# Kernel optimization log

Hardware: AMD Instinct MI355X
Metric: run time of the kernel (lower is better)

The kernel has to match this reference:

```python
import jax, jax.numpy as jnp
import numpy as np

S, B, F = 2048, 2, 1024
H, D = 16, 64
P = H * D  # packed dim = 1024


def setup_inputs() -> dict:
    key = jax.random.key(0)
    k1, k2, k3 = jax.random.split(key, 3)
    return {
        "src": jax.random.normal(k1, (S, B, F), dtype=jnp.float32),
        "in_proj_weight": jax.random.normal(k2, (3 * P, F), dtype=jnp.float32) * (1.0 / np.sqrt(F)),
        "in_proj_bias": jnp.zeros((3 * P,), dtype=jnp.float32),
        "out_proj_weight": jax.random.normal(k3, (F, P), dtype=jnp.float32) * (1.0 / np.sqrt(P)),
        "out_proj_bias": jnp.zeros((F,), dtype=jnp.float32),
    }


def reference(src, in_proj_weight, in_proj_bias, out_proj_weight, out_proj_bias):
    s, b, f = src.shape
    h, d = H, D
    # fused QKV projection: [S,B,3P]
    qkv = jnp.einsum("sbf,pf->sbp", src, in_proj_weight) + in_proj_bias
    q, k, v = jnp.split(qkv, 3, axis=-1)  # each [S,B,P]
    # [S,B,P] -> [S, B*H, D] -> [B*H, S, D]
    def to_heads(x):
        return jnp.swapaxes(x.reshape(s, b * h, d), 0, 1)
    q = to_heads(q) / np.sqrt(d)
    k = to_heads(k)
    v = to_heads(v)
    attn = jnp.einsum("nsd,ntd->nst", q, k)  # [B*H, S, S]
    attn = jax.nn.softmax(attn, axis=-1)
    out = jnp.einsum("nst,ntd->nsd", attn, v)  # [B*H, S, D]
    out = jnp.swapaxes(out, 0, 1).reshape(s * b, h * d)  # [S*B, P]
    out = out @ out_proj_weight.T + out_proj_bias  # [S*B, F]
    return out.reshape(s, b, f)
```

## Files before the change

### kernel.cpp

```cpp
#include <hip/hip_runtime.h>

#define S_LEN 2048
#define B_SZ  2
#define F_DIM 1024
#define H_N   16
#define D_DIM 64
#define P_DIM 1024
#define M_ROWS 4096
#define NBH   32

typedef __bf16 bf16x8 __attribute__((ext_vector_type(8)));
typedef __bf16 bf16x4 __attribute__((ext_vector_type(4)));
typedef float  f32x4  __attribute__((ext_vector_type(4)));
typedef unsigned short u16;
typedef unsigned short u16x8 __attribute__((ext_vector_type(8)));
typedef unsigned short u16x4 __attribute__((ext_vector_type(4)));

__device__ __forceinline__ float bf2f(u16 u) {
  union { unsigned int i; float f; } x;
  x.i = ((unsigned int)u) << 16;
  return x.f;
}
__device__ __forceinline__ u16 f2bf(float f) {
  union { float f; unsigned int i; } x;
  x.f = f;
  unsigned int u = x.i;
  u += 0x7fffu + ((u >> 16) & 1u);
  return (u16)(u >> 16);
}

__global__ __launch_bounds__(256) void cvt_all(const float* __restrict__ a,
                                               const float* __restrict__ b,
                                               const float* __restrict__ c_,
                                               u16* __restrict__ oa,
                                               u16* __restrict__ ob,
                                               u16* __restrict__ oc) {
  int i = blockIdx.x * 256 + threadIdx.x;
  const float* in;
  u16* out;
  int off;
  if (i < 1048576)      { in = a;  out = oa; off = i; }
  else if (i < 1835008) { in = b;  out = ob; off = i - 1048576; }
  else                  { in = c_; out = oc; off = i - 1835008; }
  f32x4 v = *reinterpret_cast<const f32x4*>(in + (size_t)off * 4);
  u16x4 o;
  o[0] = f2bf(v[0]); o[1] = f2bf(v[1]); o[2] = f2bf(v[2]); o[3] = f2bf(v[3]);
  *reinterpret_cast<u16x4*>(out + (size_t)off * 4) = o;
}

__device__ __forceinline__ void stage_tile(const u16* __restrict__ gbase,
                                           u16* lds, int row0, int k0,
                                           int wave, int lane) {
  #pragma unroll
  for (int i = 0; i < 2; i++) {
    const u16* g = gbase + ((size_t)(row0 + i * 64 + wave * 16 + (lane >> 2)) << 10)
                 + k0 + (lane & 3) * 8;
    u16* l = lds + (i * 64 + wave * 16) * 32;
    __builtin_amdgcn_global_load_lds(
        (const __attribute__((address_space(1))) void*)(const void*)g,
        (__attribute__((address_space(3))) void*)(void*)l, 16, 0, 0);
  }
}

__global__ __launch_bounds__(256) void qkv_gemm(const u16* __restrict__ A,
                                                const u16* __restrict__ W,
                                                const float* __restrict__ bias,
                                                u16* __restrict__ qw,
                                                u16* __restrict__ kw,
                                                u16* __restrict__ vt) {
  __shared__ u16 As[3][128 * 32];
  __shared__ u16 Bs[3][128 * 32];

  const int lane = threadIdx.x & 63;
  const int wave = threadIdx.x >> 6;
  const int wr = wave >> 1, wc = wave & 1;
  const int bm = blockIdx.y * 128;
  const int bn = blockIdx.x * 128;
  const int c = lane & 15;
  const int g = lane >> 4;

  f32x4 acc[4][4];
  #pragma unroll
  for (int mi = 0; mi < 4; mi++)
    #pragma unroll
    for (int ni = 0; ni < 4; ni++) {
      f32x4 z = {0.f, 0.f, 0.f, 0.f};
      acc[mi][ni] = z;
    }

  stage_tile(A, As[0], bm, 0, wave, lane);
  stage_tile(W, Bs[0], bn, 0, wave, lane);
  stage_tile(A, As[1], bm, 32, wave, lane);
  stage_tile(W, Bs[1], bn, 32, wave, lane);

  int cur = 0;
  for (int kt = 0; kt < 32; kt++) {
    if (kt < 31) asm volatile("s_waitcnt vmcnt(4)" ::: "memory");
    else         asm volatile("s_waitcnt vmcnt(0)" ::: "memory");
    __builtin_amdgcn_s_barrier();
    __builtin_amdgcn_sched_barrier(0);
    if (kt + 2 < 32) {
      int nb = cur + 2; if (nb >= 3) nb -= 3;
      stage_tile(A, As[nb], bm, (kt + 2) * 32, wave, lane);
      stage_tile(W, Bs[nb], bn, (kt + 2) * 32, wave, lane);
    }
    bf16x8 a[4], b[4];
    #pragma unroll
    for (int mi = 0; mi < 4; mi++)
      a[mi] = *reinterpret_cast<const bf16x8*>(&As[cur][(wr * 64 + mi * 16 + c) * 32 + g * 8]);
    #pragma unroll
    for (int ni = 0; ni < 4; ni++)
      b[ni] = *reinterpret_cast<const bf16x8*>(&Bs[cur][(wc * 64 + ni * 16 + c) * 32 + g * 8]);
    __builtin_amdgcn_s_setprio(1);
    #pragma unroll
    for (int mi = 0; mi < 4; mi++)
      #pragma unroll
      for (int ni = 0; ni < 4; ni++)
        acc[mi][ni] = __builtin_amdgcn_mfma_f32_16x16x32_bf16(a[mi], b[ni], acc[mi][ni], 0, 0, 0);
    __builtin_amdgcn_s_setprio(0);
    cur = (cur == 2) ? 0 : cur + 1;
  }

  #pragma unroll
  for (int ni = 0; ni < 4; ni++) {
    const int p = bn + wc * 64 + ni * 16 + c;
    const float bv = bias[p];
    const int which = p >> 10;
    const int pp = p & 1023;
    const int h = pp >> 6, d = pp & 63;
    const float scale = (which == 0) ? 0.125f * 1.44269504f : 1.0f;
    #pragma unroll
    for (int mi = 0; mi < 4; mi++) {
      #pragma unroll
      for (int r = 0; r < 4; r++) {
        const int m = bm + wr * 64 + mi * 16 + g * 4 + r;
        const int s = m >> 1, b_ = m & 1;
        const int n = b_ * 16 + h;
        const float v = (acc[mi][ni][r] + bv) * scale;
        const u16 hv = f2bf(v);
        if (which == 0)      qw[((size_t)n * 2048 + s) * 64 + d] = hv;
        else if (which == 1) kw[((size_t)n * 2048 + s) * 64 + d] = hv;
        else                 vt[((size_t)n * 64 + d) * 2048 + s] = hv;
      }
    }
  }
}

__global__ __launch_bounds__(256) void out_gemm(const u16* __restrict__ A,
                                                const u16* __restrict__ W,
                                                const float* __restrict__ bias,
                                                float* __restrict__ out) {
  __shared__ u16 As[3][128 * 32];
  __shared__ u16 Bs[3][128 * 32];

  const int lane = threadIdx.x & 63;
  const int wave = threadIdx.x >> 6;
  const int wr = wave >> 1, wc = wave & 1;
  const int bm = blockIdx.y * 128;
  const int bn = blockIdx.x * 128;
  const int c = lane & 15;
  const int g = lane >> 4;

  f32x4 acc[4][4];
  #pragma unroll
  for (int mi = 0; mi < 4; mi++)
    #pragma unroll
    for (int ni = 0; ni < 4; ni++) {
      f32x4 z = {0.f, 0.f, 0.f, 0.f};
      acc[mi][ni] = z;
    }

  stage_tile(A, As[0], bm, 0, wave, lane);
  stage_tile(W, Bs[0], bn, 0, wave, lane);
  stage_tile(A, As[1], bm, 32, wave, lane);
  stage_tile(W, Bs[1], bn, 32, wave, lane);

  int cur = 0;
  for (int kt = 0; kt < 32; kt++) {
    if (kt < 31) asm volatile("s_waitcnt vmcnt(4)" ::: "memory");
    else         asm volatile("s_waitcnt vmcnt(0)" ::: "memory");
    __builtin_amdgcn_s_barrier();
    __builtin_amdgcn_sched_barrier(0);
    if (kt + 2 < 32) {
      int nb = cur + 2; if (nb >= 3) nb -= 3;
      stage_tile(A, As[nb], bm, (kt + 2) * 32, wave, lane);
      stage_tile(W, Bs[nb], bn, (kt + 2) * 32, wave, lane);
    }
    bf16x8 a[4], b[4];
    #pragma unroll
    for (int mi = 0; mi < 4; mi++)
      a[mi] = *reinterpret_cast<const bf16x8*>(&As[cur][(wr * 64 + mi * 16 + c) * 32 + g * 8]);
    #pragma unroll
    for (int ni = 0; ni < 4; ni++)
      b[ni] = *reinterpret_cast<const bf16x8*>(&Bs[cur][(wc * 64 + ni * 16 + c) * 32 + g * 8]);
    __builtin_amdgcn_s_setprio(1);
    #pragma unroll
    for (int mi = 0; mi < 4; mi++)
      #pragma unroll
      for (int ni = 0; ni < 4; ni++)
        acc[mi][ni] = __builtin_amdgcn_mfma_f32_16x16x32_bf16(a[mi], b[ni], acc[mi][ni], 0, 0, 0);
    __builtin_amdgcn_s_setprio(0);
    cur = (cur == 2) ? 0 : cur + 1;
  }

  #pragma unroll
  for (int ni = 0; ni < 4; ni++) {
    const int f = bn + wc * 64 + ni * 16 + c;
    const float bv = bias[f];
    #pragma unroll
    for (int mi = 0; mi < 4; mi++) {
      #pragma unroll
      for (int r = 0; r < 4; r++) {
        const int m = bm + wr * 64 + mi * 16 + g * 4 + r;
        out[(size_t)m * 1024 + f] = acc[mi][ni][r] + bv;
      }
    }
  }
}

__device__ __forceinline__ void stage_kv(const u16* __restrict__ kb,
                                         const u16* __restrict__ vb,
                                         int ks0, u16* ksbuf, u16* vsbuf,
                                         int wave, int tid) {
  const int row = tid >> 3;
  const int scc = (tid & 7) ^ (row & 7);
  u16* lk = ksbuf + (wave * 64) * 8;
  u16* lv = vsbuf + (wave * 64) * 8;
  __builtin_amdgcn_global_load_lds(
      (const __attribute__((address_space(1))) void*)(const void*)
          (kb + (size_t)(ks0 + row) * 64 + scc * 8),
      (__attribute__((address_space(3))) void*)(void*)lk, 16, 0, 0);
  __builtin_amdgcn_global_load_lds(
      (const __attribute__((address_space(1))) void*)(const void*)
          (vb + (size_t)row * 2048 + ks0 + scc * 8),
      (__attribute__((address_space(3))) void*)(void*)lv, 16, 0, 0);
}

__global__ __launch_bounds__(512) void attn_fwd(const u16* __restrict__ qw,
                                                const u16* __restrict__ kw,
                                                const u16* __restrict__ vt,
                                                u16* __restrict__ ao) {
  __shared__ u16 Ks[3][64 * 64];
  __shared__ u16 Vs[3][64 * 64];
  __shared__ u16 Pl[8][16][76];

  const int tid = threadIdx.x;
  const int wave = tid >> 6;
  const int lane = tid & 63;
  const int c = lane & 15;
  const int g = lane >> 4;
  const int sw = c & 7;

  const int bid = blockIdx.x;
  const int id = (bid & 7) * 64 + (bid >> 3);
  const int n = id >> 4;
  const int qt = id & 15;
  const int b_ = n >> 4, h = n & 15;
  const int q0 = qt * 128 + wave * 16;

  bf16x8 qb[2];
  #pragma unroll
  for (int kk = 0; kk < 2; kk++)
    qb[kk] = *reinterpret_cast<const bf16x8*>(
        qw + ((size_t)n * 2048 + q0 + c) * 64 + kk * 32 + g * 8);

  const u16* kb = kw + (size_t)n * 2048 * 64;
  const u16* vb = vt + (size_t)n * 64 * 2048;

  f32x4 O[4];
  float l_run = 0.f;
  #pragma unroll
  for (int dt = 0; dt < 4; dt++) {
    f32x4 z = {0.f, 0.f, 0.f, 0.f};
    O[dt] = z;
  }

  stage_kv(kb, vb, 0,  Ks[0], Vs[0], wave, tid);
  stage_kv(kb, vb, 64, Ks[1], Vs[1], wave, tid);

  int cur = 0;
  for (int kt = 0; kt < 32; kt++) {
    if (kt < 31) asm volatile("s_waitcnt vmcnt(2)" ::: "memory");
    else         asm volatile("s_waitcnt vmcnt(0)" ::: "memory");
    __builtin_amdgcn_s_barrier();
    __builtin_amdgcn_sched_barrier(0);
    if (kt + 2 < 32) {
      int nb = cur + 2; if (nb >= 3) nb -= 3;
      stage_kv(kb, vb, (kt + 2) * 64, Ks[nb], Vs[nb], wave, tid);
    }

    f32x4 s[4];
    #pragma unroll
    for (int st = 0; st < 4; st++) { f32x4 z = {0.f,0.f,0.f,0.f}; s[st] = z; }
    __builtin_amdgcn_s_setprio(1);
    #pragma unroll
    for (int st = 0; st < 4; st++) {
      #pragma unroll
      for (int kk = 0; kk < 2; kk++) {
        bf16x8 ka = *reinterpret_cast<const bf16x8*>(
            &Ks[cur][(st * 16 + c) * 64 + ((kk * 4 + g) ^ sw) * 8]);
        s[st] = __builtin_amdgcn_mfma_f32_16x16x32_bf16(ka, qb[kk], s[st], 0, 0, 0);
      }
    }
    __builtin_amdgcn_s_setprio(0);

    float psum = 0.f;
    #pragma unroll
    for (int st = 0; st < 4; st++) {
      const float p0 = __builtin_amdgcn_exp2f(s[st][0]);
      const float p1 = __builtin_amdgcn_exp2f(s[st][1]);
      const float p2 = __builtin_amdgcn_exp2f(s[st][2]);
      const float p3 = __builtin_amdgcn_exp2f(s[st][3]);
      psum += (p0 + p1) + (p2 + p3);
      bf16x4 pk = { (__bf16)p0, (__bf16)p1, (__bf16)p2, (__bf16)p3 };
      *reinterpret_cast<bf16x4*>(&Pl[wave][c][st * 16 + g * 4]) = pk;
    }
    l_run += psum;

    __builtin_amdgcn_s_setprio(1);
    #pragma unroll
    for (int kk = 0; kk < 2; kk++) {
      bf16x8 pa = *reinterpret_cast<const bf16x8*>(&Pl[wave][c][kk * 32 + g * 8]);
      #pragma unroll
      for (int dt = 0; dt < 4; dt++) {
        bf16x8 vf = *reinterpret_cast<const bf16x8*>(
            &Vs[cur][(dt * 16 + c) * 64 + ((kk * 4 + g) ^ sw) * 8]);
        O[dt] = __builtin_amdgcn_mfma_f32_16x16x32_bf16(pa, vf, O[dt], 0, 0, 0);
      }
    }
    __builtin_amdgcn_s_setprio(0);

    cur = (cur == 2) ? 0 : cur + 1;
  }

  l_run += __shfl_xor(l_run, 16);
  l_run += __shfl_xor(l_run, 32);

  #pragma unroll
  for (int r = 0; r < 4; r++) {
    const float lq = __shfl(l_run, g * 4 + r);
    const float inv = 1.0f / lq;
    const int q = q0 + g * 4 + r;
    const size_t m = (size_t)q * 2 + b_;
    #pragma unroll
    for (int dt = 0; dt < 4; dt++)
      ao[m * 1024 + h * 64 + dt * 16 + c] = f2bf(O[dt][r] * inv);
  }
}

extern "C" void kernel_launch(void* const* d_in, const int* in_sizes, int n_in,
                              void* d_out, int out_size, void* d_ws, size_t ws_size,
                              hipStream_t stream) {
  const float* src   = (const float*)d_in[0];
  const float* w_in  = (const float*)d_in[1];
  const float* b_in  = (const float*)d_in[2];
  const float* w_out = (const float*)d_in[3];
  const float* b_out = (const float*)d_in[4];
  float* out = (float*)d_out;

  char* ws = (char*)d_ws;
  u16* srcb = (u16*)(ws);
  u16* wib  = (u16*)(ws + ((size_t)8  << 20));
  u16* wob  = (u16*)(ws + ((size_t)14 << 20));
  u16* qw   = (u16*)(ws + ((size_t)16 << 20));
  u16* kw   = (u16*)(ws + ((size_t)24 << 20));
  u16* vt   = (u16*)(ws + ((size_t)32 << 20));
  u16* ao   = (u16*)(ws + ((size_t)40 << 20));

  cvt_all<<<8192, 256, 0, stream>>>(src, w_in, w_out, srcb, wib, wob);

  qkv_gemm<<<dim3(24, 32), 256, 0, stream>>>(srcb, wib, b_in, qw, kw, vt);
  attn_fwd<<<512, 512, 0, stream>>>(qw, kw, vt, ao);
  out_gemm<<<dim3(8, 32), 256, 0, stream>>>(ao, wob, b_out, out);
}
```

Baseline: 123.8 us.

## Software-pipeline PV matmul one tile behind QK to overlap exp with MFMA

Restructures the attention loop so the P·V MFMAs for the previous key tile run right after the current tile's QK MFMAs, before the exp2 softmax step. A fourth V buffer keeps the previous V tile alive, and a drain step after the loop handles the last tile. The aim is to let the exp/convert VALU work overlap with matrix-core work instead of running serially. In exchange it uses more LDS, which may reduce occupancy. There is also a possible hazard: Pl is written each iteration and read in the next without an explicit barrier, which relies on the per-wave ordering.

```diff
diff --git a/kernel.cpp b/kernel.cpp
--- a/kernel.cpp
+++ b/kernel.cpp
@@ -241,7 +241,7 @@
                                                 const u16* __restrict__ vt,
                                                 u16* __restrict__ ao) {
   __shared__ u16 Ks[3][64 * 64];
-  __shared__ u16 Vs[3][64 * 64];
+  __shared__ u16 Vs[4][64 * 64];
   __shared__ u16 Pl[8][16][76];
 
   const int tid = threadIdx.x;
@@ -278,15 +278,17 @@
   stage_kv(kb, vb, 0,  Ks[0], Vs[0], wave, tid);
   stage_kv(kb, vb, 64, Ks[1], Vs[1], wave, tid);
 
-  int cur = 0;
+  int kc = 0;
+  int vc = 0;
   for (int kt = 0; kt < 32; kt++) {
     if (kt < 31) asm volatile("s_waitcnt vmcnt(2)" ::: "memory");
     else         asm volatile("s_waitcnt vmcnt(0)" ::: "memory");
     __builtin_amdgcn_s_barrier();
     __builtin_amdgcn_sched_barrier(0);
     if (kt + 2 < 32) {
-      int nb = cur + 2; if (nb >= 3) nb -= 3;
-      stage_kv(kb, vb, (kt + 2) * 64, Ks[nb], Vs[nb], wave, tid);
+      int nk = kc + 2; if (nk >= 3) nk -= 3;
+      int nv = vc + 2; if (nv >= 4) nv -= 4;
+      stage_kv(kb, vb, (kt + 2) * 64, Ks[nk], Vs[nv], wave, tid);
     }
 
     f32x4 s[4];
@@ -298,11 +300,27 @@
       #pragma unroll
       for (int kk = 0; kk < 2; kk++) {
         bf16x8 ka = *reinterpret_cast<const bf16x8*>(
-            &Ks[cur][(st * 16 + c) * 64 + ((kk * 4 + g) ^ sw) * 8]);
+            &Ks[kc][(st * 16 + c) * 64 + ((kk * 4 + g) ^ sw) * 8]);
         s[st] = __builtin_amdgcn_mfma_f32_16x16x32_bf16(ka, qb[kk], s[st], 0, 0, 0);
       }
     }
     __builtin_amdgcn_s_setprio(0);
+
+    if (kt > 0) {
+      const int pv = (vc == 0) ? 3 : vc - 1;
+      __builtin_amdgcn_s_setprio(1);
+      #pragma unroll
+      for (int kk = 0; kk < 2; kk++) {
+        bf16x8 pa = *reinterpret_cast<const bf16x8*>(&Pl[wave][c][kk * 32 + g * 8]);
+        #pragma unroll
+        for (int dt = 0; dt < 4; dt++) {
+          bf16x8 vf = *reinterpret_cast<const bf16x8*>(
+              &Vs[pv][(dt * 16 + c) * 64 + ((kk * 4 + g) ^ sw) * 8]);
+          O[dt] = __builtin_amdgcn_mfma_f32_16x16x32_bf16(pa, vf, O[dt], 0, 0, 0);
+        }
+      }
+      __builtin_amdgcn_s_setprio(0);
+    }
 
     float psum = 0.f;
     #pragma unroll
@@ -317,20 +335,22 @@
     }
     l_run += psum;
 
-    __builtin_amdgcn_s_setprio(1);
+    kc = (kc == 2) ? 0 : kc + 1;
+    vc = (vc == 3) ? 0 : vc + 1;
+  }
+
+  {
+    const int pv = 3;
     #pragma unroll
     for (int kk = 0; kk < 2; kk++) {
       bf16x8 pa = *reinterpret_cast<const bf16x8*>(&Pl[wave][c][kk * 32 + g * 8]);
       #pragma unroll
       for (int dt = 0; dt < 4; dt++) {
         bf16x8 vf = *reinterpret_cast<const bf16x8*>(
-            &Vs[cur][(dt * 16 + c) * 64 + ((kk * 4 + g) ^ sw) * 8]);
+            &Vs[pv][(dt * 16 + c) * 64 + ((kk * 4 + g) ^ sw) * 8]);
         O[dt] = __builtin_amdgcn_mfma_f32_16x16x32_bf16(pa, vf, O[dt], 0, 0, 0);
       }
     }
-    __builtin_amdgcn_s_setprio(0);
-
-    cur = (cur == 2) ? 0 : cur + 1;
   }
 
   l_run += __shfl_xor(l_run, 16);
```

Result: no change. 125.0 us (+0.9%).

## Give each attention wave 32 query rows to reuse K/V fragments, halve block size

Applied to the files above, without the earlier changes.

The attention kernel now runs 256 threads per block, and each wave handles two 16-row query sub-tiles. Each K and V fragment read from LDS therefore feeds two MFMAs, which halves LDS read traffic per FLOP. K/V staging is split into two loads per thread, and the vmcnt wait is adjusted to match. The QKV epilogue also hoists the Q/K/V selection to a block-uniform value. The cost is higher register pressure and fewer waves per block, which can reduce occupancy and latency hiding.

```diff
diff --git a/kernel.cpp b/kernel.cpp
--- a/kernel.cpp
+++ b/kernel.cpp
@@ -121,14 +121,14 @@
     cur = (cur == 2) ? 0 : cur + 1;
   }
 
+  const int which = bn >> 10;
+  const float qscale = 0.125f * 1.44269504f;
   #pragma unroll
   for (int ni = 0; ni < 4; ni++) {
     const int p = bn + wc * 64 + ni * 16 + c;
     const float bv = bias[p];
-    const int which = p >> 10;
     const int pp = p & 1023;
     const int h = pp >> 6, d = pp & 63;
-    const float scale = (which == 0) ? 0.125f * 1.44269504f : 1.0f;
     #pragma unroll
     for (int mi = 0; mi < 4; mi++) {
       #pragma unroll
@@ -136,11 +136,12 @@
         const int m = bm + wr * 64 + mi * 16 + g * 4 + r;
         const int s = m >> 1, b_ = m & 1;
         const int n = b_ * 16 + h;
-        const float v = (acc[mi][ni][r] + bv) * scale;
-        const u16 hv = f2bf(v);
-        if (which == 0)      qw[((size_t)n * 2048 + s) * 64 + d] = hv;
-        else if (which == 1) kw[((size_t)n * 2048 + s) * 64 + d] = hv;
-        else                 vt[((size_t)n * 64 + d) * 2048 + s] = hv;
+        if (which == 0)
+          qw[((size_t)n * 2048 + s) * 64 + d] = f2bf((acc[mi][ni][r] + bv) * qscale);
+        else if (which == 1)
+          kw[((size_t)n * 2048 + s) * 64 + d] = f2bf(acc[mi][ni][r] + bv);
+        else
+          vt[((size_t)n * 64 + d) * 2048 + s] = f2bf(acc[mi][ni][r] + bv);
       }
     }
   }
@@ -222,27 +223,31 @@
                                          const u16* __restrict__ vb,
                                          int ks0, u16* ksbuf, u16* vsbuf,
                                          int wave, int tid) {
-  const int row = tid >> 3;
-  const int scc = (tid & 7) ^ (row & 7);
-  u16* lk = ksbuf + (wave * 64) * 8;
-  u16* lv = vsbuf + (wave * 64) * 8;
-  __builtin_amdgcn_global_load_lds(
-      (const __attribute__((address_space(1))) void*)(const void*)
-          (kb + (size_t)(ks0 + row) * 64 + scc * 8),
-      (__attribute__((address_space(3))) void*)(void*)lk, 16, 0, 0);
-  __builtin_amdgcn_global_load_lds(
-      (const __attribute__((address_space(1))) void*)(const void*)
-          (vb + (size_t)row * 2048 + ks0 + scc * 8),
-      (__attribute__((address_space(3))) void*)(void*)lv, 16, 0, 0);
-}
-
-__global__ __launch_bounds__(512) void attn_fwd(const u16* __restrict__ qw,
+  #pragma unroll
+  for (int i = 0; i < 2; i++) {
+    const int chunk = i * 256 + tid;
+    const int row = chunk >> 3;
+    const int scc = (chunk & 7) ^ (row & 7);
+    u16* lk = ksbuf + (i * 256 + wave * 64) * 8;
+    u16* lv = vsbuf + (i * 256 + wave * 64) * 8;
+    __builtin_amdgcn_global_load_lds(
+        (const __attribute__((address_space(1))) void*)(const void*)
+            (kb + (size_t)(ks0 + row) * 64 + scc * 8),
+        (__attribute__((address_space(3))) void*)(void*)lk, 16, 0, 0);
+    __builtin_amdgcn_global_load_lds(
+        (const __attribute__((address_space(1))) void*)(const void*)
+            (vb + (size_t)row * 2048 + ks0 + scc * 8),
+        (__attribute__((address_space(3))) void*)(void*)lv, 16, 0, 0);
+  }
+}
+
+__global__ __launch_bounds__(256) void attn_fwd(const u16* __restrict__ qw,
                                                 const u16* __restrict__ kw,
                                                 const u16* __restrict__ vt,
                                                 u16* __restrict__ ao) {
   __shared__ u16 Ks[3][64 * 64];
   __shared__ u16 Vs[3][64 * 64];
-  __shared__ u16 Pl[8][16][76];
+  __shared__ u16 Pl[4][32][76];
 
   const int tid = threadIdx.x;
   const int wave = tid >> 6;
@@ -256,31 +261,35 @@
   const int n = id >> 4;
   const int qt = id & 15;
   const int b_ = n >> 4, h = n & 15;
-  const int q0 = qt * 128 + wave * 16;
-
-  bf16x8 qb[2];
-  #pragma unroll
-  for (int kk = 0; kk < 2; kk++)
-    qb[kk] = *reinterpret_cast<const bf16x8*>(
-        qw + ((size_t)n * 2048 + q0 + c) * 64 + kk * 32 + g * 8);
+  const int q0 = qt * 128 + wave * 32;
+
+  bf16x8 qb[2][2];
+  #pragma unroll
+  for (int sp = 0; sp < 2; sp++)
+    #pragma unroll
+    for (int kk = 0; kk < 2; kk++)
+      qb[sp][kk] = *reinterpret_cast<const bf16x8*>(
+          qw + ((size_t)n * 2048 + q0 + sp * 16 + c) * 64 + kk * 32 + g * 8);
 
   const u16* kb = kw + (size_t)n * 2048 * 64;
   const u16* vb = vt + (size_t)n * 64 * 2048;
 
-  f32x4 O[4];
-  float l_run = 0.f;
-  #pragma unroll
-  for (int dt = 0; dt < 4; dt++) {
-    f32x4 z = {0.f, 0.f, 0.f, 0.f};
-    O[dt] = z;
-  }
+  f32x4 O[2][4];
+  float l_run[2] = {0.f, 0.f};
+  #pragma unroll
+  for (int sp = 0; sp < 2; sp++)
+    #pragma unroll
+    for (int dt = 0; dt < 4; dt++) {
+      f32x4 z = {0.f, 0.f, 0.f, 0.f};
+      O[sp][dt] = z;
+    }
 
   stage_kv(kb, vb, 0,  Ks[0], Vs[0], wave, tid);
   stage_kv(kb, vb, 64, Ks[1], Vs[1], wave, tid);
 
   int cur = 0;
   for (int kt = 0; kt < 32; kt++) {
-    if (kt < 31) asm volatile("s_waitcnt vmcnt(2)" ::: "memory");
+    if (kt < 31) asm volatile("s_waitcnt vmcnt(4)" ::: "memory");
     else         asm volatile("s_waitcnt vmcnt(0)" ::: "memory");
     __builtin_amdgcn_s_barrier();
     __builtin_amdgcn_sched_barrier(0);
@@ -289,9 +298,11 @@
       stage_kv(kb, vb, (kt + 2) * 64, Ks[nb], Vs[nb], wave, tid);
     }
 
-    f32x4 s[4];
-    #pragma unroll
-    for (int st = 0; st < 4; st++) { f32x4 z = {0.f,0.f,0.f,0.f}; s[st] = z; }
+    f32x4 s[2][4];
+    #pragma unroll
+    for (int sp = 0; sp < 2; sp++)
+      #pragma unroll
+      for (int st = 0; st < 4; st++) { f32x4 z = {0.f,0.f,0.f,0.f}; s[sp][st] = z; }
     __builtin_amdgcn_s_setprio(1);
     #pragma unroll
     for (int st = 0; st < 4; st++) {
@@ -299,33 +310,39 @@
       for (int kk = 0; kk < 2; kk++) {
         bf16x8 ka = *reinterpret_cast<const bf16x8*>(
             &Ks[cur][(st * 16 + c) * 64 + ((kk * 4 + g) ^ sw) * 8]);
-        s[st] = __builtin_amdgcn_mfma_f32_16x16x32_bf16(ka, qb[kk], s[st], 0, 0, 0);
+        s[0][st] = __builtin_amdgcn_mfma_f32_16x16x32_bf16(ka, qb[0][kk], s[0][st], 0, 0, 0);
+        s[1][st] = __builtin_amdgcn_mfma_f32_16x16x32_bf16(ka, qb[1][kk], s[1][st], 0, 0, 0);
       }
     }
     __builtin_amdgcn_s_setprio(0);
 
-    float psum = 0.f;
-    #pragma unroll
-    for (int st = 0; st < 4; st++) {
-      const float p0 = __builtin_amdgcn_exp2f(s[st][0]);
-      const float p1 = __builtin_amdgcn_exp2f(s[st][1]);
-      const float p2 = __builtin_amdgcn_exp2f(s[st][2]);
-      const float p3 = __builtin_amdgcn_exp2f(s[st][3]);
-      psum += (p0 + p1) + (p2 + p3);
-      bf16x4 pk = { (__bf16)p0, (__bf16)p1, (__bf16)p2, (__bf16)p3 };
-      *reinterpret_cast<bf16x4*>(&Pl[wave][c][st * 16 + g * 4]) = pk;
-    }
-    l_run += psum;
+    #pragma unroll
+    for (int sp = 0; sp < 2; sp++) {
+      float psum = 0.f;
+      #pragma unroll
+      for (int st = 0; st < 4; st++) {
+        const float p0 = __builtin_amdgcn_exp2f(s[sp][st][0]);
+        const float p1 = __builtin_amdgcn_exp2f(s[sp][st][1]);
+        const float p2 = __builtin_amdgcn_exp2f(s[sp][st][2]);
+        const float p3 = __builtin_amdgcn_exp2f(s[sp][st][3]);
+        psum += (p0 + p1) + (p2 + p3);
+        bf16x4 pk = { (__bf16)p0, (__bf16)p1, (__bf16)p2, (__bf16)p3 };
+        *reinterpret_cast<bf16x4*>(&Pl[wave][sp * 16 + c][st * 16 + g * 4]) = pk;
+      }
+      l_run[sp] += psum;
+    }
 
     __builtin_amdgcn_s_setprio(1);
     #pragma unroll
     for (int kk = 0; kk < 2; kk++) {
-      bf16x8 pa = *reinterpret_cast<const bf16x8*>(&Pl[wave][c][kk * 32 + g * 8]);
+      bf16x8 pa0 = *reinterpret_cast<const bf16x8*>(&Pl[wave][ 0 + c][kk * 32 + g * 8]);
+      bf16x8 pa1 = *reinterpret_cast<const bf16x8*>(&Pl[wave][16 + c][kk * 32 + g * 8]);
       #pragma unroll
       for (int dt = 0; dt < 4; dt++) {
         bf16x8 vf = *reinterpret_cast<const bf16x8*>(
             &Vs[cur][(dt * 16 + c) * 64 + ((kk * 4 + g) ^ sw) * 8]);
-        O[dt] = __builtin_amdgcn_mfma_f32_16x16x32_bf16(pa, vf, O[dt], 0, 0, 0);
+        O[0][dt] = __builtin_amdgcn_mfma_f32_16x16x32_bf16(pa0, vf, O[0][dt], 0, 0, 0);
+        O[1][dt] = __builtin_amdgcn_mfma_f32_16x16x32_bf16(pa1, vf, O[1][dt], 0, 0, 0);
       }
     }
     __builtin_amdgcn_s_setprio(0);
@@ -333,18 +350,21 @@
     cur = (cur == 2) ? 0 : cur + 1;
   }
 
-  l_run += __shfl_xor(l_run, 16);
-  l_run += __shfl_xor(l_run, 32);
-
-  #pragma unroll
-  for (int r = 0; r < 4; r++) {
-    const float lq = __shfl(l_run, g * 4 + r);
-    const float inv = 1.0f / lq;
-    const int q = q0 + g * 4 + r;
-    const size_t m = (size_t)q * 2 + b_;
-    #pragma unroll
-    for (int dt = 0; dt < 4; dt++)
-      ao[m * 1024 + h * 64 + dt * 16 + c] = f2bf(O[dt][r] * inv);
+  #pragma unroll
+  for (int sp = 0; sp < 2; sp++) {
+    float lt = l_run[sp];
+    lt += __shfl_xor(lt, 16);
+    lt += __shfl_xor(lt, 32);
+    #pragma unroll
+    for (int r = 0; r < 4; r++) {
+      const float lq = __shfl(lt, g * 4 + r);
+      const float inv = 1.0f / lq;
+      const int q = q0 + sp * 16 + g * 4 + r;
+      const size_t m = (size_t)q * 2 + b_;
+      #pragma unroll
+      for (int dt = 0; dt < 4; dt++)
+        ao[m * 1024 + h * 64 + dt * 16 + c] = f2bf(O[sp][dt][r] * inv);
+    }
   }
 }
 
@@ -370,6 +390,6 @@
   cvt_all<<<8192, 256, 0, stream>>>(src, w_in, w_out, srcb, wib, wob);
 
   qkv_gemm<<<dim3(24, 32), 256, 0, stream>>>(srcb, wib, b_in, qw, kw, vt);
-  attn_fwd<<<512, 512, 0, stream>>>(qw, kw, vt, ao);
+  attn_fwd<<<512, 256, 0, stream>>>(qw, kw, vt, ao);
   out_gemm<<<dim3(8, 32), 256, 0, stream>>>(ao, wob, b_out, out);
 }
```

After: 131.7 us. 1.06x slower.

## Enlarge QKV GEMM tiles to 256x256x64 with swizzled LDS and block remap

Applied to the files above, without the earlier changes.

Restructures the QKV projection GEMM to use 256x256 output tiles with K-step 64, 512 threads (8 waves in a 2x4 layout), and double buffering in place of the earlier triple buffering. LDS rows are XOR-swizzled to avoid bank conflicts, and block IDs are remapped so neighbouring blocks share rows of A for L2 reuse. The aim is higher arithmetic intensity and fewer global loads per MFMA. The costs are 128KB of LDS, a one-block-per-CU limit, only 192 blocks on the machine, and a full vmcnt(0) wait each iteration that may expose load latency.

```diff
diff --git a/kernel.cpp b/kernel.cpp
--- a/kernel.cpp
+++ b/kernel.cpp
@@ -62,85 +62,121 @@
   }
 }
 
-__global__ __launch_bounds__(256) void qkv_gemm(const u16* __restrict__ A,
+__device__ __forceinline__ void stage_tile64(const u16* __restrict__ gbase,
+                                             u16* lds, int row0, int k0,
+                                             int wave, int tid) {
+  #pragma unroll
+  for (int i = 0; i < 4; i++) {
+    const int chunk = i * 512 + tid;
+    const int row = chunk >> 3;
+    const int scc = (chunk & 7) ^ (row & 7);
+    u16* l = lds + (i * 512 + wave * 64) * 8;
+    __builtin_amdgcn_global_load_lds(
+        (const __attribute__((address_space(1))) void*)(const void*)
+            (gbase + (size_t)(row0 + row) * 1024 + k0 + scc * 8),
+        (__attribute__((address_space(3))) void*)(void*)l, 16, 0, 0);
+  }
+}
+
+__global__ __launch_bounds__(512) void qkv_gemm(const u16* __restrict__ A,
                                                 const u16* __restrict__ W,
                                                 const float* __restrict__ bias,
                                                 u16* __restrict__ qw,
                                                 u16* __restrict__ kw,
                                                 u16* __restrict__ vt) {
-  __shared__ u16 As[3][128 * 32];
-  __shared__ u16 Bs[3][128 * 32];
-
-  const int lane = threadIdx.x & 63;
-  const int wave = threadIdx.x >> 6;
-  const int wr = wave >> 1, wc = wave & 1;
-  const int bm = blockIdx.y * 128;
-  const int bn = blockIdx.x * 128;
+  __shared__ u16 As[2][256 * 64];
+  __shared__ u16 Bs[2][256 * 64];
+
+  const int tid = threadIdx.x;
+  const int lane = tid & 63;
+  const int wave = tid >> 6;
+  const int wr = wave >> 2;
+  const int wc = wave & 3;
   const int c = lane & 15;
   const int g = lane >> 4;
-
-  f32x4 acc[4][4];
-  #pragma unroll
-  for (int mi = 0; mi < 4; mi++)
+  const int sw = c & 7;
+
+  const int bid = blockIdx.x;
+  const int id = (bid & 7) * 24 + (bid >> 3);
+  const int bm = (id / 12) * 256;
+  const int bn = (id % 12) * 256;
+
+  f32x4 acc[8][4];
+  #pragma unroll
+  for (int mi = 0; mi < 8; mi++)
     #pragma unroll
     for (int ni = 0; ni < 4; ni++) {
       f32x4 z = {0.f, 0.f, 0.f, 0.f};
       acc[mi][ni] = z;
     }
 
-  stage_tile(A, As[0], bm, 0, wave, lane);
-  stage_tile(W, Bs[0], bn, 0, wave, lane);
-  stage_tile(A, As[1], bm, 32, wave, lane);
-  stage_tile(W, Bs[1], bn, 32, wave, lane);
+  stage_tile64(A, As[0], bm, 0, wave, tid);
+  stage_tile64(W, Bs[0], bn, 0, wave, tid);
+  asm volatile("s_waitcnt vmcnt(0)" ::: "memory");
+  __builtin_amdgcn_s_barrier();
 
   int cur = 0;
-  for (int kt = 0; kt < 32; kt++) {
-    if (kt < 31) asm volatile("s_waitcnt vmcnt(4)" ::: "memory");
-    else         asm volatile("s_waitcnt vmcnt(0)" ::: "memory");
+  for (int kt = 0; kt < 16; kt++) {
+    if (kt < 15) {
+      stage_tile64(A, As[cur ^ 1], bm, (kt + 1) * 64, wave, tid);
+      stage_tile64(W, Bs[cur ^ 1], bn, (kt + 1) * 64, wave, tid);
+    }
+    #pragma unroll
+    for (int mh = 0; mh < 2; mh++) {
+      bf16x8 a[4][2];
+      #pragma unroll
+      for (int mi = 0; mi < 4; mi++)
+        #pragma unroll
+        for (int kk = 0; kk < 2; kk++)
+          a[mi][kk] = *reinterpret_cast<const bf16x8*>(
+              &As[cur][(wr * 128 + (mh * 4 + mi) * 16 + c) * 64 + (((kk * 4 + g) ^ sw) * 8)]);
+      #pragma unroll
+      for (int nh = 0; nh < 2; nh++) {
+        bf16x8 b[2][2];
+        #pragma unroll
+        for (int ni = 0; ni < 2; ni++)
+          #pragma unroll
+          for (int kk = 0; kk < 2; kk++)
+            b[ni][kk] = *reinterpret_cast<const bf16x8*>(
+                &Bs[cur][(wc * 64 + (nh * 2 + ni) * 16 + c) * 64 + (((kk * 4 + g) ^ sw) * 8)]);
+        __builtin_amdgcn_s_setprio(1);
+        #pragma unroll
+        for (int mi = 0; mi < 4; mi++)
+          #pragma unroll
+          for (int ni = 0; ni < 2; ni++)
+            #pragma unroll
+            for (int kk = 0; kk < 2; kk++)
+              acc[mh * 4 + mi][nh * 2 + ni] = __builtin_amdgcn_mfma_f32_16x16x32_bf16(
+                  a[mi][kk], b[ni][kk], acc[mh * 4 + mi][nh * 2 + ni], 0, 0, 0);
+        __builtin_amdgcn_s_setprio(0);
+      }
+    }
+    asm volatile("s_waitcnt vmcnt(0)" ::: "memory");
     __builtin_amdgcn_s_barrier();
-    __builtin_amdgcn_sched_barrier(0);
-    if (kt + 2 < 32) {
-      int nb = cur + 2; if (nb >= 3) nb -= 3;
-      stage_tile(A, As[nb], bm, (kt + 2) * 32, wave, lane);
-      stage_tile(W, Bs[nb], bn, (kt + 2) * 32, wave, lane);
-    }
-    bf16x8 a[4], b[4];
-    #pragma unroll
-    for (int mi = 0; mi < 4; mi++)
-      a[mi] = *reinterpret_cast<const bf16x8*>(&As[cur][(wr * 64 + mi * 16 + c) * 32 + g * 8]);
-    #pragma unroll
-    for (int ni = 0; ni < 4; ni++)
-      b[ni] = *reinterpret_cast<const bf16x8*>(&Bs[cur][(wc * 64 + ni * 16 + c) * 32 + g * 8]);
-    __builtin_amdgcn_s_setprio(1);
-    #pragma unroll
-    for (int mi = 0; mi < 4; mi++)
-      #pragma unroll
-      for (int ni = 0; ni < 4; ni++)
-        acc[mi][ni] = __builtin_amdgcn_mfma_f32_16x16x32_bf16(a[mi], b[ni], acc[mi][ni], 0, 0, 0);
-    __builtin_amdgcn_s_setprio(0);
-    cur = (cur == 2) ? 0 : cur + 1;
-  }
-
+    cur ^= 1;
+  }
+
+  const int which = bn >> 10;
+  const float qscale = 0.125f * 1.44269504f;
   #pragma unroll
   for (int ni = 0; ni < 4; ni++) {
     const int p = bn + wc * 64 + ni * 16 + c;
     const float bv = bias[p];
-    const int which = p >> 10;
     const int pp = p & 1023;
     const int h = pp >> 6, d = pp & 63;
-    const float scale = (which == 0) ? 0.125f * 1.44269504f : 1.0f;
-    #pragma unroll
-    for (int mi = 0; mi < 4; mi++) {
+    #pragma unroll
+    for (int mi = 0; mi < 8; mi++) {
       #pragma unroll
       for (int r = 0; r < 4; r++) {
-        const int m = bm + wr * 64 + mi * 16 + g * 4 + r;
+        const int m = bm + wr * 128 + mi * 16 + g * 4 + r;
         const int s = m >> 1, b_ = m & 1;
         const int n = b_ * 16 + h;
-        const float v = (acc[mi][ni][r] + bv) * scale;
-        const u16 hv = f2bf(v);
-        if (which == 0)      qw[((size_t)n * 2048 + s) * 64 + d] = hv;
-        else if (which == 1) kw[((size_t)n * 2048 + s) * 64 + d] = hv;
-        else                 vt[((size_t)n * 64 + d) * 2048 + s] = hv;
+        if (which == 0)
+          qw[((size_t)n * 2048 + s) * 64 + d] = f2bf((acc[mi][ni][r] + bv) * qscale);
+        else if (which == 1)
+          kw[((size_t)n * 2048 + s) * 64 + d] = f2bf(acc[mi][ni][r] + bv);
+        else
+          vt[((size_t)n * 64 + d) * 2048 + s] = f2bf(acc[mi][ni][r] + bv);
       }
     }
   }
@@ -369,7 +405,7 @@
 
   cvt_all<<<8192, 256, 0, stream>>>(src, w_in, w_out, srcb, wib, wob);
 
-  qkv_gemm<<<dim3(24, 32), 256, 0, stream>>>(srcb, wib, b_in, qw, kw, vt);
+  qkv_gemm<<<192, 512, 0, stream>>>(srcb, wib, b_in, qw, kw, vt);
   attn_fwd<<<512, 512, 0, stream>>>(qw, kw, vt, ao);
   out_gemm<<<dim3(8, 32), 256, 0, stream>>>(ao, wob, b_out, out);
 }
```

Measured after the change: 143.4 us. 15.8% more time.
